# Optimization experiments

Measured on AMD Instinct MI355X. Metric: run time of the kernel, lower is better.

## Reference

```python
import jax, jax.numpy as jnp
import numpy as np

N_FULL, N_SUB, NNZ = 100000, 32768, 1048576
F_IN, DH, DOUT = 512, 512, 512
EPS_NORM = 1e-9   # HighOrderAggregator 'norm' bias eps
EPS_L2 = 1e-12    # F.normalize eps


def spmm(row, col, val, feat, n):
    # sparse [n,n] @ dense [n,d] via gather + segment-sum scatter
    return jax.ops.segment_sum(val[:, None] * feat[col], row, num_segments=n)


def ho_layer(row, col, val, feat, Ws, bs, scales, offsets, n):
    # HighOrderAggregator, order=1, act=relu, bias='norm', aggr='concat'
    hops = [feat, spmm(row, col, val, feat, n)]
    parts = []
    for h, W, b, s, o in zip(hops, Ws, bs, scales, offsets):
        f = jax.nn.relu(h @ W.T + b)
        mean = jnp.mean(f, axis=1, keepdims=True)
        var = jnp.var(f, axis=1, keepdims=True)  # unbiased=False, matches torch
        parts.append((f - mean) * s * jax.lax.rsqrt(var + EPS_NORM) + o)
    return jnp.concatenate(parts, axis=1)


def _xavier(k, shape):
    fan_out, fan_in = shape
    lim = float(np.sqrt(6.0 / (fan_in + fan_out)))
    return jax.random.uniform(k, shape, jnp.float32, -lim, lim)


def setup_inputs() -> dict:
    key = jax.random.key(0)
    ks = jax.random.split(key, 24)
    inp = {}
    inp['feat_full'] = jax.random.normal(ks[0], (N_FULL, F_IN), jnp.float32)
    inp['node_subgraph'] = jax.random.randint(ks[1], (N_SUB,), 0, N_FULL)
    inp['adj_row'] = jax.random.randint(ks[2], (NNZ,), 0, N_SUB)
    inp['adj_col'] = jax.random.randint(ks[3], (NNZ,), 0, N_SUB)
    inp['adj_val'] = jax.random.uniform(ks[4], (NNZ,), jnp.float32)
    # layer 1: dim_in=512 -> 512 per order, concat -> 1024
    inp['W1_0'] = _xavier(ks[5], (DH, F_IN))
    inp['W1_1'] = _xavier(ks[6], (DH, F_IN))
    inp['b1_0'] = 0.02 * jax.random.normal(ks[7], (DH,), jnp.float32)
    inp['b1_1'] = 0.02 * jax.random.normal(ks[8], (DH,), jnp.float32)
    inp['s1_0'] = 1.0 + 0.1 * jax.random.normal(ks[9], (DH,), jnp.float32)
    inp['s1_1'] = 1.0 + 0.1 * jax.random.normal(ks[10], (DH,), jnp.float32)
    inp['o1_0'] = 0.02 * jax.random.normal(ks[11], (DH,), jnp.float32)
    inp['o1_1'] = 0.02 * jax.random.normal(ks[12], (DH,), jnp.float32)
    # layer 2: dim_in=1024 -> 512 per order, concat -> 1024
    inp['W2_0'] = _xavier(ks[13], (DH, 2 * DH))
    inp['W2_1'] = _xavier(ks[14], (DH, 2 * DH))
    inp['b2_0'] = 0.02 * jax.random.normal(ks[15], (DH,), jnp.float32)
    inp['b2_1'] = 0.02 * jax.random.normal(ks[16], (DH,), jnp.float32)
    inp['s2_0'] = 1.0 + 0.1 * jax.random.normal(ks[17], (DH,), jnp.float32)
    inp['s2_1'] = 1.0 + 0.1 * jax.random.normal(ks[18], (DH,), jnp.float32)
    inp['o2_0'] = 0.02 * jax.random.normal(ks[19], (DH,), jnp.float32)
    inp['o2_1'] = 0.02 * jax.random.normal(ks[20], (DH,), jnp.float32)
    # classifier: order=0, act='I', bias='bias'
    inp['Wc'] = _xavier(ks[21], (DOUT, 2 * DH))
    inp['bc'] = 0.02 * jax.random.normal(ks[22], (DOUT,), jnp.float32)
    return inp


def reference(feat_full, node_subgraph, adj_row, adj_col, adj_val,
              W1_0, W1_1, b1_0, b1_1, s1_0, s1_1, o1_0, o1_1,
              W2_0, W2_1, b2_0, b2_1, s2_0, s2_1, o2_0, o2_1,
              Wc, bc):
    feat = feat_full[node_subgraph]                       # [N_SUB, F_IN] gather
    h = ho_layer(adj_row, adj_col, adj_val, feat,
                 (W1_0, W1_1), (b1_0, b1_1), (s1_0, s1_1), (o1_0, o1_1), N_SUB)
    h = ho_layer(adj_row, adj_col, adj_val, h,
                 (W2_0, W2_1), (b2_0, b2_1), (s2_0, s2_1), (o2_0, o2_1), N_SUB)
    nrm = jnp.linalg.norm(h, axis=1, keepdims=True)       # F.normalize p=2 dim=1
    h = h / jnp.maximum(nrm, EPS_L2)
    return h @ Wc.T + bc                                  # classifier (act='I')
```

## Files before the change

kernel.cpp:

```cpp
#include <hip/hip_runtime.h>
#include <stdint.h>

typedef unsigned short u16;
typedef unsigned int u32;

#define NSUB 32768
#define NNZ_E 1048576

using short8 = __attribute__((ext_vector_type(8))) short;
using f32x4  = __attribute__((ext_vector_type(4))) float;

__device__ __forceinline__ u16 f2b(float f) {
  u32 u = __float_as_uint(f);
  return (u16)((u + 0x7fffu + ((u >> 16) & 1u)) >> 16);
}
__device__ __forceinline__ float b2f(u16 x) {
  return __uint_as_float(((u32)x) << 16);
}

__device__ __forceinline__ void glds16(const void* g, void* l) {
  __builtin_amdgcn_global_load_lds(
      (const __attribute__((address_space(1))) u32*)g,
      (__attribute__((address_space(3))) u32*)l, 16, 0, 0);
}

#define GATHER_B 16384
#define COUNT_B 4096
__global__ __launch_bounds__(256) void u_prep(
    const float* __restrict__ ff, const int* __restrict__ idx, u16* __restrict__ FEAT,
    const int* __restrict__ arow, const int* __restrict__ acol, int* __restrict__ cnt8,
    const float* W1_0, const float* W1_1, const float* W2_0, const float* W2_1,
    const float* Wc, u16* W1_0b, u16* W1_1b, u16* W2cat, u16* Wcb) {
  int bid = blockIdx.x, t = threadIdx.x;
  if (bid < GATHER_B) {
    int r = bid * 2 + (t >> 7);
    int c = (t & 127) * 4;
    size_t src = (size_t)idx[r];
    float4 v = *(const float4*)(ff + src * 512 + c);
    ushort4 o;
    o.x = f2b(v.x); o.y = f2b(v.y); o.z = f2b(v.z); o.w = f2b(v.w);
    *(ushort4*)(FEAT + (size_t)r * 512 + c) = o;
  } else if (bid < GATHER_B + COUNT_B) {
    int i = (bid - GATHER_B) * 256 + t;
    atomicAdd(&cnt8[arow[i] * 8 + (acol[i] >> 12)], 1);
  } else {
    int cid = bid - GATHER_B - COUNT_B;
    const float* src; u16* dst; int i;
    if (cid < 256)       { src = W1_0; dst = W1_0b;              i = cid * 256 + t; }
    else if (cid < 512)  { src = W1_1; dst = W1_1b;              i = (cid - 256) * 256 + t; }
    else if (cid < 1024) { src = W2_0; dst = W2cat;              i = (cid - 512) * 256 + t; }
    else if (cid < 1536) { src = W2_1; dst = W2cat + 512 * 1024; i = (cid - 1024) * 256 + t; }
    else                 { src = Wc;   dst = Wcb;                i = (cid - 1536) * 256 + t; }
    float4 v = ((const float4*)src)[i];
    ushort4 o;
    o.x = f2b(v.x); o.y = f2b(v.y); o.z = f2b(v.z); o.w = f2b(v.w);
    ((ushort4*)dst)[i] = o;
  }
}

__global__ __launch_bounds__(256) void scan_part(const int* __restrict__ cnt8,
                                                 int* __restrict__ bsum) {
  int bid = blockIdx.x, t = threadIdx.x;
  int4 c = *(const int4*)(cnt8 + bid * 1024 + t * 4);
  int s = c.x + c.y + c.z + c.w;
#pragma unroll
  for (int d = 1; d < 64; d <<= 1) s += __shfl_xor(s, d);
  __shared__ int red[4];
  if ((t & 63) == 0) red[t >> 6] = s;
  __syncthreads();
  if (t == 0) bsum[bid] = red[0] + red[1] + red[2] + red[3];
}

__global__ __launch_bounds__(256) void scan_top(const int* __restrict__ bsum,
                                                int* __restrict__ boff) {
  int t = threadIdx.x;
  int v = bsum[t];
  int s = v;
#pragma unroll
  for (int d = 1; d < 64; d <<= 1) {
    int u = __shfl_up(s, d);
    if ((t & 63) >= d) s += u;
  }
  __shared__ int wsum[4];
  if ((t & 63) == 63) wsum[t >> 6] = s;
  __syncthreads();
  int add = 0;
  for (int w = 0; w < (t >> 6); ++w) add += wsum[w];
  boff[t] = s + add - v;
}

__global__ __launch_bounds__(256) void scan_final(const int* __restrict__ cnt8,
                                                  const int* __restrict__ boff,
                                                  int* __restrict__ off,
                                                  int* __restrict__ cursor8) {
  int bid = blockIdx.x, t = threadIdx.x;
  int base = bid * 1024 + t * 4;
  int4 c = *(const int4*)(cnt8 + base);
  int s = c.x + c.y + c.z + c.w;
  int inc = s;
#pragma unroll
  for (int d = 1; d < 64; d <<= 1) {
    int u = __shfl_up(inc, d);
    if ((t & 63) >= d) inc += u;
  }
  __shared__ int wsum[4];
  if ((t & 63) == 63) wsum[t >> 6] = inc;
  __syncthreads();
  int add = 0;
  for (int w = 0; w < (t >> 6); ++w) add += wsum[w];
  int run = boff[bid] + inc + add - s;
  int vals[4] = {c.x, c.y, c.z, c.w};
#pragma unroll
  for (int j = 0; j < 4; ++j) {
    int idx = base + j;
    cursor8[idx] = run;
    if ((idx & 7) == 0) off[idx >> 3] = run;
    run += vals[j];
  }
  if (bid == 255 && t == 255) off[NSUB] = run;
}

__global__ __launch_bounds__(256) void edge_scatter8(const int* __restrict__ row,
                                                     const int* __restrict__ col,
                                                     const float* __restrict__ val,
                                                     int* __restrict__ cursor8,
                                                     int2* __restrict__ cv) {
  int i = blockIdx.x * 256 + threadIdx.x;
  int c = col[i];
  int p = atomicAdd(&cursor8[row[i] * 8 + (c >> 12)], 1);
  int2 e; e.x = c; e.y = __float_as_int(val[i]);
  cv[p] = e;
}

__device__ __forceinline__ void norm_rowstore(float* a, int lane, int r,
                                              const float* __restrict__ bias,
                                              const float* __restrict__ sc,
                                              const float* __restrict__ ofs,
                                              u16* __restrict__ Y, int ldy, int col_off) {
  float4 b0 = *(const float4*)(bias + lane * 8);
  float4 b1 = *(const float4*)(bias + lane * 8 + 4);
  a[0] = fmaxf(a[0] + b0.x, 0.f); a[1] = fmaxf(a[1] + b0.y, 0.f);
  a[2] = fmaxf(a[2] + b0.z, 0.f); a[3] = fmaxf(a[3] + b0.w, 0.f);
  a[4] = fmaxf(a[4] + b1.x, 0.f); a[5] = fmaxf(a[5] + b1.y, 0.f);
  a[6] = fmaxf(a[6] + b1.z, 0.f); a[7] = fmaxf(a[7] + b1.w, 0.f);
  float sum = 0.f, sq = 0.f;
#pragma unroll
  for (int j = 0; j < 8; ++j) { sum += a[j]; sq += a[j] * a[j]; }
#pragma unroll
  for (int d = 1; d < 64; d <<= 1) {
    sum += __shfl_xor(sum, d);
    sq  += __shfl_xor(sq, d);
  }
  float mean = sum * (1.f / 512.f);
  float var = sq * (1.f / 512.f) - mean * mean;
  float rstd = rsqrtf(var + 1e-9f);
  float4 s0 = *(const float4*)(sc + lane * 8);
  float4 s1 = *(const float4*)(sc + lane * 8 + 4);
  float4 o0 = *(const float4*)(ofs + lane * 8);
  float4 o1 = *(const float4*)(ofs + lane * 8 + 4);
  int4 o;
  o.x = (int)((u32)f2b((a[0] - mean) * s0.x * rstd + o0.x) |
              ((u32)f2b((a[1] - mean) * s0.y * rstd + o0.y) << 16));
  o.y = (int)((u32)f2b((a[2] - mean) * s0.z * rstd + o0.z) |
              ((u32)f2b((a[3] - mean) * s0.w * rstd + o0.w) << 16));
  o.z = (int)((u32)f2b((a[4] - mean) * s1.x * rstd + o1.x) |
              ((u32)f2b((a[5] - mean) * s1.y * rstd + o1.y) << 16));
  o.w = (int)((u32)f2b((a[6] - mean) * s1.z * rstd + o1.z) |
              ((u32)f2b((a[7] - mean) * s1.w * rstd + o1.w) << 16));
  *(int4*)(Y + (size_t)r * ldy + col_off + lane * 8) = o;
}

__device__ __forceinline__ void fma8(int4 u, float v, float* a) {
  u32 w;
  w = (u32)u.x; a[0] += v * __uint_as_float(w << 16); a[1] += v * __uint_as_float(w & 0xffff0000u);
  w = (u32)u.y; a[2] += v * __uint_as_float(w << 16); a[3] += v * __uint_as_float(w & 0xffff0000u);
  w = (u32)u.z; a[4] += v * __uint_as_float(w << 16); a[5] += v * __uint_as_float(w & 0xffff0000u);
  w = (u32)u.w; a[6] += v * __uint_as_float(w << 16); a[7] += v * __uint_as_float(w & 0xffff0000u);
}

template <int LDX, bool NORM>
__device__ __forceinline__ void spmm_dev(const int* __restrict__ off,
                                         const int2* __restrict__ cv,
                                         const u16* __restrict__ X,
                                         u16* __restrict__ Y, int ldy, int col_off,
                                         const float* __restrict__ bias,
                                         const float* __restrict__ sc,
                                         const float* __restrict__ ofs, int bid) {
  const int lane = threadIdx.x & 63, wave = threadIdx.x >> 6;
  const int r = bid * 4 + wave;
  const int s = __builtin_amdgcn_readfirstlane(off[r]);
  const int e = __builtin_amdgcn_readfirstlane(off[r + 1]);
  float a[8] = {0.f, 0.f, 0.f, 0.f, 0.f, 0.f, 0.f, 0.f};
  const u16* Xl = X + lane * 8;
  int i = s;
  for (; i + 4 <= e; i += 4) {
    int2 p0 = cv[i], p1 = cv[i + 1], p2 = cv[i + 2], p3 = cv[i + 3];
    int4 u0 = *(const int4*)(Xl + (size_t)p0.x * LDX);
    int4 u1 = *(const int4*)(Xl + (size_t)p1.x * LDX);
    int4 u2 = *(const int4*)(Xl + (size_t)p2.x * LDX);
    int4 u3 = *(const int4*)(Xl + (size_t)p3.x * LDX);
    fma8(u0, __int_as_float(p0.y), a);
    fma8(u1, __int_as_float(p1.y), a);
    fma8(u2, __int_as_float(p2.y), a);
    fma8(u3, __int_as_float(p3.y), a);
  }
  for (; i < e; ++i) {
    int2 p0 = cv[i];
    int4 u0 = *(const int4*)(Xl + (size_t)p0.x * LDX);
    fma8(u0, __int_as_float(p0.y), a);
  }
  if (NORM) {
    norm_rowstore(a, lane, r, bias, sc, ofs, Y, ldy, col_off);
  } else {
    int4 o;
    o.x = (int)((u32)f2b(a[0]) | ((u32)f2b(a[1]) << 16));
    o.y = (int)((u32)f2b(a[2]) | ((u32)f2b(a[3]) << 16));
    o.z = (int)((u32)f2b(a[4]) | ((u32)f2b(a[5]) << 16));
    o.w = (int)((u32)f2b(a[6]) | ((u32)f2b(a[7]) << 16));
    *(int4*)(Y + (size_t)r * ldy + col_off + lane * 8) = o;
  }
}

__global__ __launch_bounds__(256) void spmm1_k(const int* __restrict__ off,
                                               const int2* __restrict__ cv,
                                               const u16* __restrict__ X,
                                               u16* __restrict__ Y) {
  spmm_dev<512, false>(off, cv, X, Y, 512, 0, nullptr, nullptr, nullptr, blockIdx.x);
}

__device__ __forceinline__ void rownorm_dev(const u16* __restrict__ F, int ldf,
                                            const float* __restrict__ bias,
                                            const float* __restrict__ sc,
                                            const float* __restrict__ ofs,
                                            u16* __restrict__ Y, int ldy, int col_off,
                                            int bid) {
  const int lane = threadIdx.x & 63, wave = threadIdx.x >> 6;
  const int r = bid * 4 + wave;
  int4 u = *(const int4*)(F + (size_t)r * ldf + lane * 8);
  float a[8];
  a[0] = __uint_as_float(((u32)u.x) << 16); a[1] = __uint_as_float(((u32)u.x) & 0xffff0000u);
  a[2] = __uint_as_float(((u32)u.y) << 16); a[3] = __uint_as_float(((u32)u.y) & 0xffff0000u);
  a[4] = __uint_as_float(((u32)u.z) << 16); a[5] = __uint_as_float(((u32)u.z) & 0xffff0000u);
  a[6] = __uint_as_float(((u32)u.w) << 16); a[7] = __uint_as_float(((u32)u.w) & 0xffff0000u);
  norm_rowstore(a, lane, r, bias, sc, ofs, Y, ldy, col_off);
}

__global__ __launch_bounds__(256) void rownorm_k(const u16* __restrict__ F, int ldf,
                                                 const float* __restrict__ bias,
                                                 const float* __restrict__ sc,
                                                 const float* __restrict__ ofs,
                                                 u16* __restrict__ Y, int col_off) {
  rownorm_dev(F, ldf, bias, sc, ofs, Y, 1024, col_off, blockIdx.x);
}

__global__ __launch_bounds__(256) void u_l2(const int* __restrict__ row_off,
                                            const int2* __restrict__ cv,
                                            const u16* __restrict__ TTL,
                                            u16* __restrict__ H2,
                                            const float* __restrict__ b2_0,
                                            const float* __restrict__ s2_0,
                                            const float* __restrict__ o2_0,
                                            const float* __restrict__ b2_1,
                                            const float* __restrict__ s2_1,
                                            const float* __restrict__ o2_1) {
  int bid = blockIdx.x;
  if (bid < 8192)
    spmm_dev<1024, true>(row_off, cv, TTL + 512, H2, 1024, 512, b2_1, s2_1, o2_1, bid);
  else
    rownorm_dev(TTL, 1024, b2_0, s2_0, o2_0, H2, 1024, 0, bid - 8192);
}

template <int K, int LDC, bool BIAS, bool BF16OUT, bool RS>
__global__ __launch_bounds__(256) void gemm_bt(const u16* __restrict__ A,
                                               const u16* __restrict__ W,
                                               const float* __restrict__ bias,
                                               const float* __restrict__ rs,
                                               float* __restrict__ Cf,
                                               u16* __restrict__ Cb) {
  __shared__ __align__(16) u16 As[128 * 32];
  __shared__ __align__(16) u16 Bs[128 * 32];
  const int t = threadIdx.x;
  const int lane = t & 63, wave = t >> 6;
  const int wm = (wave >> 1) * 64, wn = (wave & 1) * 64;
  const int nwg = gridDim.x * gridDim.y;
  const int bid = blockIdx.x + gridDim.x * blockIdx.y;
  const int sbid = (bid % 8) * (nwg / 8) + bid / 8;
  const int bx = sbid % gridDim.x, by = sbid / gridDim.x;
  const int m0 = by * 128, n0 = bx * 128;

  f32x4 acc[4][4];
#pragma unroll
  for (int m = 0; m < 4; ++m)
#pragma unroll
    for (int n = 0; n < 4; ++n) acc[m][n] = f32x4{0.f, 0.f, 0.f, 0.f};

  const int lr = t >> 2;
  const int lc = (t & 3) * 8;
  const u16* Ag  = A + (size_t)(m0 + lr) * K + lc;
  const u16* Ag2 = Ag + (size_t)64 * K;
  const u16* Wg  = W + (size_t)(n0 + lr) * K + lc;
  const u16* Wg2 = Wg + (size_t)64 * K;
  char* asb0 = (char*)As + wave * 1024;
  char* asb1 = (char*)As + 4096 + wave * 1024;
  char* bsb0 = (char*)Bs + wave * 1024;
  char* bsb1 = (char*)Bs + 4096 + wave * 1024;
  const int fr = lane & 15, kh = lane >> 4;

  for (int kt = 0; kt < K / 32; ++kt) {
    glds16(Ag + kt * 32, asb0);
    glds16(Ag2 + kt * 32, asb1);
    glds16(Wg + kt * 32, bsb0);
    glds16(Wg2 + kt * 32, bsb1);
    __syncthreads();
    short8 af[4], bfr[4];
#pragma unroll
    for (int m = 0; m < 4; ++m)
      af[m] = *(const short8*)&As[(wm + m * 16 + fr) * 32 + kh * 8];
#pragma unroll
    for (int n = 0; n < 4; ++n)
      bfr[n] = *(const short8*)&Bs[(wn + n * 16 + fr) * 32 + kh * 8];
#pragma unroll
    for (int m = 0; m < 4; ++m)
#pragma unroll
      for (int n = 0; n < 4; ++n)
        acc[m][n] = __builtin_amdgcn_mfma_f32_16x16x32_bf16(af[m], bfr[n], acc[m][n], 0, 0, 0);
    __syncthreads();
  }

  const int crow = (lane >> 4) * 4;
  const int ccol = lane & 15;
#pragma unroll
  for (int n = 0; n < 4; ++n) {
    int col = n0 + wn + n * 16 + ccol;
    float bv = BIAS ? bias[col] : 0.f;
#pragma unroll
    for (int m = 0; m < 4; ++m) {
      int row = m0 + wm + m * 16 + crow;
#pragma unroll
      for (int q = 0; q < 4; ++q) {
        float v = acc[m][n][q];
        if (RS) v *= rs[row + q];
        v += bv;
        if (BF16OUT)
          Cb[(size_t)(row + q) * LDC + col] = f2b(v);
        else
          Cf[(size_t)(row + q) * LDC + col] = v;
      }
    }
  }
}

__global__ __launch_bounds__(256) void l2scale(const u16* __restrict__ H,
                                               float* __restrict__ rn) {
  const int lane = threadIdx.x & 63, wave = threadIdx.x >> 6;
  const int r = blockIdx.x * 4 + wave;
  const u16* row = H + (size_t)r * 1024 + lane * 16;
  int4 u0 = *(const int4*)row;
  int4 u1 = *(const int4*)(row + 8);
  float sq = 0.f;
  const int vals[8] = {u0.x, u0.y, u0.z, u0.w, u1.x, u1.y, u1.z, u1.w};
#pragma unroll
  for (int j = 0; j < 8; ++j) {
    u32 wv = (u32)vals[j];
    float f0 = __uint_as_float(wv << 16);
    float f1 = __uint_as_float(wv & 0xffff0000u);
    sq += f0 * f0 + f1 * f1;
  }
#pragma unroll
  for (int d = 1; d < 64; d <<= 1) sq += __shfl_xor(sq, d);
  if (lane == 0) rn[r] = 1.f / fmaxf(sqrtf(sq), 1e-12f);
}

extern "C" void kernel_launch(void* const* d_in, const int* in_sizes, int n_in,
                              void* d_out, int out_size, void* d_ws, size_t ws_size,
                              hipStream_t stream) {
  (void)in_sizes; (void)n_in; (void)out_size; (void)ws_size;
  const float* feat_full = (const float*)d_in[0];
  const int*   nodes = (const int*)d_in[1];
  const int*   arow = (const int*)d_in[2];
  const int*   acol = (const int*)d_in[3];
  const float* aval = (const float*)d_in[4];
  const float* W1_0 = (const float*)d_in[5];
  const float* W1_1 = (const float*)d_in[6];
  const float* b1_0 = (const float*)d_in[7];
  const float* b1_1 = (const float*)d_in[8];
  const float* s1_0 = (const float*)d_in[9];
  const float* s1_1 = (const float*)d_in[10];
  const float* o1_0 = (const float*)d_in[11];
  const float* o1_1 = (const float*)d_in[12];
  const float* W2_0 = (const float*)d_in[13];
  const float* W2_1 = (const float*)d_in[14];
  const float* b2_0 = (const float*)d_in[15];
  const float* b2_1 = (const float*)d_in[16];
  const float* s2_0 = (const float*)d_in[17];
  const float* s2_1 = (const float*)d_in[18];
  const float* o2_0 = (const float*)d_in[19];
  const float* o2_1 = (const float*)d_in[20];
  const float* Wc = (const float*)d_in[21];
  const float* bc = (const float*)d_in[22];
  float* out = (float*)d_out;

  const size_t MB = (size_t)1 << 20;
  char* p = (char*)d_ws;
  u16* FEAT = (u16*)p;
  u16* S1   = (u16*)(p + 32 * MB);
  u16* H1   = (u16*)(p + 64 * MB);
  u16* H2   = (u16*)(p + 128 * MB);
  u16* TMPb = (u16*)(p + 192 * MB);
  u16* TTL  = (u16*)(p + 192 * MB);
  u16* W1_0b = (u16*)(p + 256 * MB);
  u16* W1_1b = W1_0b + 512 * 512;
  u16* W2cat = W1_1b + 512 * 512;
  u16* Wcb   = W2cat + 1024 * 1024;
  int* row_off = (int*)(p + 260 * MB);
  int* cnt8    = (int*)(p + 261 * MB);
  int* cursor8 = (int*)(p + 262 * MB);
  float* RN    = (float*)(p + 263 * MB);
  int* bsum    = (int*)((char*)RN + 256 * 1024);
  int* boff    = bsum + 256;
  int2* cv     = (int2*)(p + 264 * MB);

  hipMemsetAsync(cnt8, 0, NSUB * 8 * sizeof(int), stream);

  u_prep<<<GATHER_B + COUNT_B + 2048, 256, 0, stream>>>(
      feat_full, nodes, FEAT, arow, acol, cnt8,
      W1_0, W1_1, W2_0, W2_1, Wc, W1_0b, W1_1b, W2cat, Wcb);

  scan_part<<<256, 256, 0, stream>>>(cnt8, bsum);
  scan_top<<<1, 256, 0, stream>>>(bsum, boff);
  scan_final<<<256, 256, 0, stream>>>(cnt8, boff, row_off, cursor8);
  edge_scatter8<<<NNZ_E / 256, 256, 0, stream>>>(arow, acol, aval, cursor8, cv);

  spmm1_k<<<NSUB / 4, 256, 0, stream>>>(row_off, cv, FEAT, S1);
  gemm_bt<512, 512, false, true, false><<<dim3(4, 256), 256, 0, stream>>>(
      FEAT, W1_0b, nullptr, nullptr, nullptr, TMPb);
  rownorm_k<<<NSUB / 4, 256, 0, stream>>>(TMPb, 512, b1_0, s1_0, o1_0, H1, 0);
  gemm_bt<512, 512, false, true, false><<<dim3(4, 256), 256, 0, stream>>>(
      S1, W1_1b, nullptr, nullptr, nullptr, TMPb);
  rownorm_k<<<NSUB / 4, 256, 0, stream>>>(TMPb, 512, b1_1, s1_1, o1_1, H1, 512);

  gemm_bt<1024, 1024, false, true, false><<<dim3(8, 256), 256, 0, stream>>>(
      H1, W2cat, nullptr, nullptr, nullptr, TTL);
  u_l2<<<8192 + 8192, 256, 0, stream>>>(row_off, cv, TTL, H2,
                                        b2_0, s2_0, o2_0, b2_1, s2_1, o2_1);

  l2scale<<<NSUB / 4, 256, 0, stream>>>(H2, RN);
  gemm_bt<1024, 512, true, false, true><<<dim3(4, 256), 256, 0, stream>>>(
      H2, Wcb, bc, RN, out, nullptr);
}
```

Measured before the change: 655.2 us.

## Co-schedule layer-1 SpMM with independent FEAT×W1_0 GEMM in one launch

Merges the first-layer SpMM and the independent FEAT@W1_0 GEMM into a single kernel, with block ranges dispatched to either a copied MFMA GEMM body or the SpMM body. The gather-bound SpMM and the compute-bound GEMM can then overlap on the GPU, and one launch is removed. The GEMM output goes to a separate temp buffer so both row-norms can run after the second GEMM. This costs extra workspace, and the combined kernel's register and LDS use is set by the GEMM path, which may lower SpMM occupancy.

```diff
diff --git a/kernel.cpp b/kernel.cpp
--- a/kernel.cpp
+++ b/kernel.cpp
@@ -221,13 +221,6 @@
   }
 }
 
-__global__ __launch_bounds__(256) void spmm1_k(const int* __restrict__ off,
-                                               const int2* __restrict__ cv,
-                                               const u16* __restrict__ X,
-                                               u16* __restrict__ Y) {
-  spmm_dev<512, false>(off, cv, X, Y, 512, 0, nullptr, nullptr, nullptr, blockIdx.x);
-}
-
 __device__ __forceinline__ void rownorm_dev(const u16* __restrict__ F, int ldf,
                                             const float* __restrict__ bias,
                                             const float* __restrict__ sc,
@@ -251,6 +244,83 @@
                                                  const float* __restrict__ ofs,
                                                  u16* __restrict__ Y, int col_off) {
   rownorm_dev(F, ldf, bias, sc, ofs, Y, 1024, col_off, blockIdx.x);
+}
+
+__global__ __launch_bounds__(256) void u_l1a(const int* __restrict__ row_off,
+                                             const int2* __restrict__ cv,
+                                             const u16* __restrict__ FEAT,
+                                             u16* __restrict__ S1,
+                                             const u16* __restrict__ W1_0b,
+                                             u16* __restrict__ TMPa) {
+  if (blockIdx.x >= 1024) {
+    spmm_dev<512, false>(row_off, cv, FEAT, S1, 512, 0, nullptr, nullptr, nullptr,
+                         blockIdx.x - 1024);
+    return;
+  }
+  __shared__ __align__(16) u16 As[128 * 32];
+  __shared__ __align__(16) u16 Bs[128 * 32];
+  const int K = 512, LDC = 512;
+  const int t = threadIdx.x;
+  const int lane = t & 63, wave = t >> 6;
+  const int wm = (wave >> 1) * 64, wn = (wave & 1) * 64;
+  const int nwg = 1024;
+  const int bid = blockIdx.x;
+  const int sbid = (bid % 8) * (nwg / 8) + bid / 8;
+  const int bx = sbid % 4, by = sbid / 4;
+  const int m0 = by * 128, n0 = bx * 128;
+
+  f32x4 acc[4][4];
+#pragma unroll
+  for (int m = 0; m < 4; ++m)
+#pragma unroll
+    for (int n = 0; n < 4; ++n) acc[m][n] = f32x4{0.f, 0.f, 0.f, 0.f};
+
+  const int lr = t >> 2;
+  const int lc = (t & 3) * 8;
+  const u16* Ag  = FEAT + (size_t)(m0 + lr) * K + lc;
+  const u16* Ag2 = Ag + (size_t)64 * K;
+  const u16* Wg  = W1_0b + (size_t)(n0 + lr) * K + lc;
+  const u16* Wg2 = Wg + (size_t)64 * K;
+  char* asb0 = (char*)As + wave * 1024;
+  char* asb1 = (char*)As + 4096 + wave * 1024;
+  char* bsb0 = (char*)Bs + wave * 1024;
+  char* bsb1 = (char*)Bs + 4096 + wave * 1024;
+  const int fr = lane & 15, kh = lane >> 4;
+
+  for (int kt = 0; kt < K / 32; ++kt) {
+    glds16(Ag + kt * 32, asb0);
+    glds16(Ag2 + kt * 32, asb1);
+    glds16(Wg + kt * 32, bsb0);
+    glds16(Wg2 + kt * 32, bsb1);
+    __syncthreads();
+    short8 af[4], bfr[4];
+#pragma unroll
+    for (int m = 0; m < 4; ++m)
+      af[m] = *(const short8*)&As[(wm + m * 16 + fr) * 32 + kh * 8];
+#pragma unroll
+    for (int n = 0; n < 4; ++n)
+      bfr[n] = *(const short8*)&Bs[(wn + n * 16 + fr) * 32 + kh * 8];
+#pragma unroll
+    for (int m = 0; m < 4; ++m)
+#pragma unroll
+      for (int n = 0; n < 4; ++n)
+        acc[m][n] = __builtin_amdgcn_mfma_f32_16x16x32_bf16(af[m], bfr[n], acc[m][n], 0, 0, 0);
+    __syncthreads();
+  }
+
+  const int crow = (lane >> 4) * 4;
+  const int ccol = lane & 15;
+#pragma unroll
+  for (int n = 0; n < 4; ++n) {
+    int col = n0 + wn + n * 16 + ccol;
+#pragma unroll
+    for (int m = 0; m < 4; ++m) {
+      int row = m0 + wm + m * 16 + crow;
+#pragma unroll
+      for (int q = 0; q < 4; ++q)
+        TMPa[(size_t)(row + q) * LDC + col] = f2b(acc[m][n][q]);
+    }
+  }
 }
 
 __global__ __launch_bounds__(256) void u_l2(const int* __restrict__ row_off,
@@ -406,7 +476,8 @@
   u16* S1   = (u16*)(p + 32 * MB);
   u16* H1   = (u16*)(p + 64 * MB);
   u16* H2   = (u16*)(p + 128 * MB);
-  u16* TMPb = (u16*)(p + 192 * MB);
+  u16* TMPa = (u16*)(p + 192 * MB);
+  u16* TMPb = (u16*)(p + 224 * MB);
   u16* TTL  = (u16*)(p + 192 * MB);
   u16* W1_0b = (u16*)(p + 256 * MB);
   u16* W1_1b = W1_0b + 512 * 512;
@@ -431,12 +502,10 @@
   scan_final<<<256, 256, 0, stream>>>(cnt8, boff, row_off, cursor8);
   edge_scatter8<<<NNZ_E / 256, 256, 0, stream>>>(arow, acol, aval, cursor8, cv);
 
-  spmm1_k<<<NSUB / 4, 256, 0, stream>>>(row_off, cv, FEAT, S1);
-  gemm_bt<512, 512, false, true, false><<<dim3(4, 256), 256, 0, stream>>>(
-      FEAT, W1_0b, nullptr, nullptr, nullptr, TMPb);
-  rownorm_k<<<NSUB / 4, 256, 0, stream>>>(TMPb, 512, b1_0, s1_0, o1_0, H1, 0);
+  u_l1a<<<1024 + 8192, 256, 0, stream>>>(row_off, cv, FEAT, S1, W1_0b, TMPa);
   gemm_bt<512, 512, false, true, false><<<dim3(4, 256), 256, 0, stream>>>(
       S1, W1_1b, nullptr, nullptr, nullptr, TMPb);
+  rownorm_k<<<NSUB / 4, 256, 0, stream>>>(TMPa, 512, b1_0, s1_0, o1_0, H1, 0);
   rownorm_k<<<NSUB / 4, 256, 0, stream>>>(TMPb, 512, b1_1, s1_1, o1_1, H1, 512);
 
   gemm_bt<1024, 1024, false, true, false><<<dim3(8, 256), 256, 0, stream>>>(
```

After: 639.1 us. 1.03x faster.
